# Kernel optimization log

Measured on AMD Instinct MI355X. Metric: run time of the kernel, lower is better.

## Reference

```python
import jax, jax.numpy as jnp
import numpy as np

B, S, F, H = 4, 1024, 256, 8
SCALE = float(F) ** 0.5  # source MULTIPLIES logits by sqrt(f)


def setup_inputs() -> dict:
    key = jax.random.key(0)
    ks = jax.random.split(key, 5)
    # 0.02 init scale keeps sigmoid logits in a non-saturated range
    return {
        "q_input": jax.random.normal(ks[0], (B, S, F), dtype=jnp.float32),
        "Wq": jax.random.normal(ks[1], (F, F * H), dtype=jnp.float32) * 0.02,
        "Wk": jax.random.normal(ks[2], (F, F * H), dtype=jnp.float32) * 0.02,
        "Wv": jax.random.normal(ks[3], (F, F * H), dtype=jnp.float32) * 0.02,
        "Wo": jax.random.normal(ks[4], (F * H, F), dtype=jnp.float32) * 0.02,
    }


def reference(q_input, Wq, Wk, Wv, Wo):
    b, s, f = q_input.shape
    h = Wq.shape[1] // f
    # kv_input is None in source -> self-attention (kv = q_input)
    q = (q_input.reshape(b * s, f) @ Wq).reshape(b, s, f, h)
    k = (q_input.reshape(b * s, f) @ Wk).reshape(b, s, f, h)
    v = (q_input.reshape(b * s, f) @ Wv).reshape(b, s, f, h)
    qkt = jnp.einsum('bifh,bjfh->bijh', q, k)          # [b, i, j, h]
    attn = jax.nn.sigmoid(qkt * SCALE)                  # sigmoid, NOT softmax
    wv = jnp.einsum('bijh,bjfh->bifh', attn, v)         # [b, i, f, h]
    wv = wv.reshape(b * s, f * h)
    out = jax.nn.relu(wv @ Wo)                          # projection + ReLU
    return out.reshape(b, s, f)
```

## Files before the change

### kernel.cpp

```cpp
#include <hip/hip_runtime.h>
#include <math.h>

#define SQ 1024
#define FQ 256
#define FH 2048

typedef _Float16 f16;
typedef f16  f16x8 __attribute__((ext_vector_type(8)));
typedef float f32x4 __attribute__((ext_vector_type(4)));

#define GLOAD_LDS16(gp, lp) \
    __builtin_amdgcn_global_load_lds((const __attribute__((address_space(1))) void*)(gp), \
                                     (__attribute__((address_space(3))) void*)(lp), 16, 0, 0)

#define SIG16(s) __builtin_amdgcn_rcpf(1.0f + __builtin_amdgcn_exp2f(-23.083120654223414f * (s)))

__global__ __launch_bounds__(256) void prep_kernel(const float* __restrict__ x,
                                                   const float* __restrict__ Wq,
                                                   const float* __restrict__ Wk,
                                                   const float* __restrict__ Wv,
                                                   const float* __restrict__ Wo,
                                                   f16* __restrict__ xh,
                                                   f16* __restrict__ wqT,
                                                   f16* __restrict__ wkT,
                                                   f16* __restrict__ wvT,
                                                   f16* __restrict__ woT) {
    const int z = blockIdx.z;
    if (z == 4) {
        int id = (int)(blockIdx.x * 8 + blockIdx.y);
        int idx = (id * 256 + (int)threadIdx.x) * 8;
        float4 a = *(const float4*)(x + idx);
        float4 b = *(const float4*)(x + idx + 4);
        f16x8 v = {(f16)a.x, (f16)a.y, (f16)a.z, (f16)a.w,
                   (f16)b.x, (f16)b.y, (f16)b.z, (f16)b.w};
        *(f16x8*)(xh + idx) = v;
        return;
    }
    __shared__ f16 T[32][33];
    const int tx = threadIdx.x & 31, ty = threadIdx.x >> 5;
    if (z < 3) {
        const float* W = z == 0 ? Wq : (z == 1 ? Wk : Wv);
        f16* WT        = z == 0 ? wqT : (z == 1 ? wkT : wvT);
        const int n0 = blockIdx.x * 32, k0 = blockIdx.y * 32;
#pragma unroll
        for (int i = 0; i < 4; ++i)
            T[ty + i * 8][tx] = (f16)W[(size_t)(k0 + ty + i * 8) * FH + n0 + tx];
        __syncthreads();
#pragma unroll
        for (int i = 0; i < 4; ++i)
            WT[(size_t)(n0 + ty + i * 8) * FQ + k0 + tx] = T[tx][ty + i * 8];
    } else {
        const int n0 = (blockIdx.x >> 3) * 32;
        const int yy = (blockIdx.x & 7) * 8 + blockIdx.y;
        const int ft = yy >> 3, h = yy & 7;
#pragma unroll
        for (int i = 0; i < 4; ++i) {
            int fl = ty + i * 8;
            T[fl][tx] = (f16)Wo[(size_t)((ft * 32 + fl) * 8 + h) * FQ + n0 + tx];
        }
        __syncthreads();
#pragma unroll
        for (int i = 0; i < 4; ++i)
            woT[(size_t)(n0 + ty + i * 8) * FH + h * 256 + ft * 32 + tx] = T[tx][ty + i * 8];
    }
}

__device__ __forceinline__ void stage_sw64(const f16* __restrict__ G, int ldg,
                                           int row0, int c0, f16* S,
                                           int nrows, int w, int lane) {
    const int rsub = lane >> 3;
    const int g    = (lane & 7) ^ (rsub & 7);
#pragma unroll
    for (int rI = w; rI < (nrows >> 3); rI += 4) {
        GLOAD_LDS16(G + (size_t)(row0 + rI * 8 + rsub) * ldg + c0 + g * 8,
                    S + rI * 512);
    }
}

__device__ __forceinline__ void gemm128_sw(const f16* __restrict__ A, int lda,
                                           const f16* __restrict__ Bt, int ldb,
                                           int kbeg, int kend, f16* As, f16* Bs,
                                           f32x4 acc[4][4], int row0, int col0) {
    const int t = threadIdx.x, lane = t & 63, w = t >> 6;
    const int wr = w >> 1, wc = w & 1;
    const int lrow = lane & 15, quad = lane >> 4;
    for (int k0 = kbeg; k0 < kend; k0 += 64) {
        __syncthreads();
        stage_sw64(A, lda, row0, k0, As, 128, w, lane);
        stage_sw64(Bt, ldb, col0, k0, Bs, 128, w, lane);
        __syncthreads();
#pragma unroll
        for (int kk = 0; kk < 2; ++kk) {
            f16x8 af[4], bf[4];
#pragma unroll
            for (int i = 0; i < 4; ++i) {
                int r = wr * 64 + i * 16 + lrow;
                af[i] = *(const f16x8*)&As[r * 64 + (((kk * 4 + quad) ^ (r & 7)) << 3)];
            }
#pragma unroll
            for (int j = 0; j < 4; ++j) {
                int r = wc * 64 + j * 16 + lrow;
                bf[j] = *(const f16x8*)&Bs[r * 64 + (((kk * 4 + quad) ^ (r & 7)) << 3)];
            }
#pragma unroll
            for (int i = 0; i < 4; ++i)
#pragma unroll
                for (int j = 0; j < 4; ++j)
                    acc[i][j] = __builtin_amdgcn_mfma_f32_16x16x32_f16(af[i], bf[j], acc[i][j], 0, 0, 0);
        }
    }
}

__global__ __launch_bounds__(256) void proj_mfma(const f16* __restrict__ xh,
                                                 const f16* __restrict__ wqT,
                                                 const f16* __restrict__ wkT,
                                                 const f16* __restrict__ wvT,
                                                 f16* __restrict__ qb,
                                                 f16* __restrict__ kb,
                                                 f16* __restrict__ vb) {
    const int z = blockIdx.z;
    const f16* WT = z == 0 ? wqT : (z == 1 ? wkT : wvT);
    f16* O        = z == 0 ? qb  : (z == 1 ? kb  : vb);
    __shared__ f16 smem[17408];
    f16* As = smem;
    f16* Bs = smem + 8192;
    f32x4 acc[4][4] = {};
    const int row0 = blockIdx.y * 128, col0 = blockIdx.x * 128;
    gemm128_sw(xh, FQ, WT, FQ, 0, FQ, As, Bs, acc, row0, col0);

    __syncthreads();
    f16* Es = smem;
    const int lane = threadIdx.x & 63, w = threadIdx.x >> 6;
    const int wr = w >> 1, wc = w & 1;
    const int lrow = lane & 15, quad = lane >> 4;
    if (z != 2) {
#pragma unroll
        for (int i = 0; i < 4; ++i)
#pragma unroll
            for (int rr = 0; rr < 4; ++rr) {
                int rl = 64 * wr + 16 * i + 4 * quad + rr;
#pragma unroll
                for (int j = 0; j < 4; ++j) {
                    int cc = 64 * wc + 16 * j + lrow;
                    Es[rl * 136 + (cc & 7) * 16 + (cc >> 3)] = (f16)acc[i][j][rr];
                }
            }
        __syncthreads();
        const int f0 = col0 >> 3;
#pragma unroll
        for (int it = 0; it < 4; ++it) {
            int c = it * 256 + threadIdx.x;
            int row = c >> 3, hh = c & 7;
            int gr = row0 + row, bbb = gr >> 10, s = gr & 1023;
            f16x8 v0 = *(const f16x8*)&Es[row * 136 + hh * 16];
            f16x8 v1 = *(const f16x8*)&Es[row * 136 + hh * 16 + 8];
            f16* dst = O + ((size_t)(bbb * 8 + hh) * SQ + s) * FQ + f0;
            *(f16x8*)dst = v0;
            *(f16x8*)(dst + 8) = v1;
        }
    } else {
#pragma unroll
        for (int i = 0; i < 4; ++i)
#pragma unroll
            for (int rr = 0; rr < 4; ++rr) {
                int rl = 64 * wr + 16 * i + 4 * quad + rr;
#pragma unroll
                for (int j = 0; j < 4; ++j) {
                    int cc = 64 * wc + 16 * j + lrow;
                    Es[cc * 136 + rl] = (f16)acc[i][j][rr];
                }
            }
        __syncthreads();
        const int bbb = row0 >> 10, s0 = row0 & 1023;
#pragma unroll
        for (int it = 0; it < 8; ++it) {
            int c = it * 256 + threadIdx.x;
            int cc = c >> 4, sc = c & 15;
            int hh = cc & 7, f = (col0 >> 3) + (cc >> 3);
            f16x8 v = *(const f16x8*)&Es[cc * 136 + sc * 8];
            *(f16x8*)(O + ((size_t)(bbb * 8 + hh) * FQ + f) * SQ + s0 + sc * 8) = v;
        }
    }
}

__global__ __launch_bounds__(256, 1) void fused_attn(const f16* __restrict__ Qb,
                                                     const f16* __restrict__ Kb,
                                                     const f16* __restrict__ Vt,
                                                     f16* __restrict__ WV) {
    __shared__ f16 smem[37888];
    const int t = threadIdx.x, lane = t & 63, w = t >> 6;
    const int lrow = lane & 15, quad = lane >> 4;
    f16* Pw = smem + 32768 + w * 1280;
    const int n = blockIdx.x;
    const int xcd = n & 7, rest = n >> 3;
    const int bh = xcd * 4 + (rest & 3);
    const int strip = rest >> 2;
    const int m0 = strip * 128;
    const int bb = bh >> 3, h = bh & 7;
    const f16* Qg = Qb + (size_t)bh * SQ * FQ;
    const f16* Kg = Kb + (size_t)bh * SQ * FQ;
    const f16* Vg = Vt + (size_t)bh * FQ * SQ;

    f16x8 qf[2][8];
#pragma unroll
    for (int mi = 0; mi < 2; ++mi)
#pragma unroll
        for (int ks = 0; ks < 8; ++ks)
            qf[mi][ks] = *(const f16x8*)(Qg + (size_t)(m0 + 32 * w + 16 * mi + lrow) * FQ
                                             + ks * 32 + quad * 8);

    const int krs = lane >> 5;
    const int kgp = lane & 31;
    const int vrs = lane >> 2;
    const int vgp = lane & 3;

#pragma unroll
    for (int i = 0; i < 4; ++i) {
        int rI = w + i * 4;
        int r = rI * 2 + krs;
        GLOAD_LDS16(Kg + (size_t)r * FQ + ((kgp ^ (r & 7)) << 3), smem + rI * 512);
    }
#pragma unroll
    for (int i = 0; i < 4; ++i) {
        int rI = w + i * 4;
        int f = rI * 16 + vrs;
        GLOAD_LDS16(Vg + (size_t)f * SQ + ((vgp ^ ((f >> 1) & 3)) << 3),
                    smem + 16384 + rI * 512);
    }

    f32x4 acc_o[2][16] = {};

    for (int jt = 0; jt < 32; ++jt) {
        const int j0 = jt * 32;
        f16* KBc = (jt & 1) ? smem + 8192  : smem;
        f16* VBc = (jt & 1) ? smem + 24576 : smem + 16384;
        __syncthreads();
        if (jt < 31) {
            f16* KBn = (jt & 1) ? smem         : smem + 8192;
            f16* VBn = (jt & 1) ? smem + 16384 : smem + 24576;
#pragma unroll
            for (int i = 0; i < 4; ++i) {
                int rI = w + i * 4;
                int r = rI * 2 + krs;
                GLOAD_LDS16(Kg + (size_t)(j0 + 32 + r) * FQ + ((kgp ^ (r & 7)) << 3),
                            KBn + rI * 512);
            }
#pragma unroll
            for (int i = 0; i < 4; ++i) {
                int rI = w + i * 4;
                int f = rI * 16 + vrs;
                GLOAD_LDS16(Vg + (size_t)f * SQ + j0 + 32 + ((vgp ^ ((f >> 1) & 3)) << 3),
                            VBn + rI * 512);
            }
        }
        f32x4 acc_s[2][2] = {};
#pragma unroll
        for (int ks = 0; ks < 8; ++ks) {
            f16x8 bf[2];
#pragma unroll
            for (int nj = 0; nj < 2; ++nj) {
                int rk = 16 * nj + lrow;
                bf[nj] = *(const f16x8*)&KBc[rk * 256 + (((ks * 4 + quad) ^ (rk & 7)) << 3)];
            }
#pragma unroll
            for (int mi = 0; mi < 2; ++mi)
#pragma unroll
                for (int nj = 0; nj < 2; ++nj)
                    acc_s[mi][nj] = __builtin_amdgcn_mfma_f32_16x16x32_f16(
                        qf[mi][ks], bf[nj], acc_s[mi][nj], 0, 0, 0);
        }
#pragma unroll
        for (int mi = 0; mi < 2; ++mi)
#pragma unroll
            for (int nj = 0; nj < 2; ++nj)
#pragma unroll
                for (int rr = 0; rr < 4; ++rr)
                    Pw[(16 * mi + 4 * quad + rr) * 40 + 16 * nj + lrow] =
                        (f16)SIG16(acc_s[mi][nj][rr]);
        f16x8 ap[2];
#pragma unroll
        for (int mi = 0; mi < 2; ++mi)
            ap[mi] = *(const f16x8*)&Pw[(16 * mi + lrow) * 40 + quad * 8];
#pragma unroll
        for (int nj = 0; nj < 16; ++nj) {
            int f = 16 * nj + lrow;
            f16x8 bv = *(const f16x8*)&VBc[f * 32 + ((quad ^ ((f >> 1) & 3)) << 3)];
#pragma unroll
            for (int mi = 0; mi < 2; ++mi)
                acc_o[mi][nj] = __builtin_amdgcn_mfma_f32_16x16x32_f16(
                    ap[mi], bv, acc_o[mi][nj], 0, 0, 0);
        }
    }
    __syncthreads();
    f16* Es = smem;
#pragma unroll
    for (int mi = 0; mi < 2; ++mi)
#pragma unroll
        for (int nj = 0; nj < 16; ++nj)
#pragma unroll
            for (int rr = 0; rr < 4; ++rr)
                Es[(32 * w + 16 * mi + 4 * quad + rr) * 264 + 16 * nj + lrow] =
                    (f16)acc_o[mi][nj][rr];
    __syncthreads();
#pragma unroll
    for (int it = 0; it < 16; ++it) {
        int c = it * 256 + t;
        int r = c >> 5, ck = c & 31;
        f16x8 v = *(const f16x8*)&Es[r * 264 + ck * 8];
        *(f16x8*)(WV + (size_t)(bb * SQ + m0 + r) * FH + h * 256 + ck * 8) = v;
    }
}

__global__ __launch_bounds__(256) void out_mfma8(const f16* __restrict__ WVm,
                                                 const f16* __restrict__ WoT,
                                                 float* __restrict__ PP) {
    __shared__ f16 smem[16384];
    f16* As = smem;
    f16* Bs = smem + 8192;
    f32x4 acc[4][4] = {};
    const int row0 = blockIdx.y * 128, col0 = blockIdx.x * 128;
    const int kbeg = blockIdx.z * 256;
    gemm128_sw(WVm, FH, WoT, FH, kbeg, kbeg + 256, As, Bs, acc, row0, col0);

    float* P = PP + (size_t)blockIdx.z * SQ * 4 * FQ;
    const int lane = threadIdx.x & 63, w = threadIdx.x >> 6;
    const int wr = w >> 1, wc = w & 1;
    const int lrow = lane & 15, quad = lane >> 4;
#pragma unroll
    for (int i = 0; i < 4; ++i)
#pragma unroll
        for (int rr = 0; rr < 4; ++rr) {
            int gr = row0 + wr * 64 + i * 16 + quad * 4 + rr;
#pragma unroll
            for (int j = 0; j < 4; ++j) {
                int gc = col0 + wc * 64 + j * 16 + lrow;
                P[(size_t)gr * FQ + gc] = acc[i][j][rr];
            }
        }
}

__global__ __launch_bounds__(256) void reduce_relu8(const float* __restrict__ PP,
                                                    float* __restrict__ O) {
    int idx = (blockIdx.x * 256 + threadIdx.x) * 4;
    f32x4 s = *(const f32x4*)(PP + idx);
#pragma unroll
    for (int z = 1; z < 8; ++z)
        s += *(const f32x4*)(PP + (size_t)z * 1048576 + idx);
    f32x4 r = {fmaxf(s.x, 0.f), fmaxf(s.y, 0.f), fmaxf(s.z, 0.f), fmaxf(s.w, 0.f)};
    *(f32x4*)(O + idx) = r;
}

extern "C" void kernel_launch(void* const* d_in, const int* in_sizes, int n_in,
                              void* d_out, int out_size, void* d_ws, size_t ws_size,
                              hipStream_t stream) {
    const float* x  = (const float*)d_in[0];
    const float* Wq = (const float*)d_in[1];
    const float* Wk = (const float*)d_in[2];
    const float* Wv = (const float*)d_in[3];
    const float* Wo = (const float*)d_in[4];
    float* out = (float*)d_out;

    f16* ws = (f16*)d_ws;
    f16* xh    = ws;
    f16* wqT   = xh    + 1048576;
    f16* wkT   = wqT   + 524288;
    f16* wvT   = wkT   + 524288;
    f16* woT   = wvT   + 524288;
    f16* qbuf  = woT   + 524288;
    f16* kbuf  = qbuf  + 8388608;
    f16* vbuf  = kbuf  + 8388608;
    f16* wvbuf = vbuf  + 8388608;
    float* pp  = (float*)qbuf;

    dim3 blk(256);
    prep_kernel<<<dim3(64, 8, 5), blk, 0, stream>>>(x, Wq, Wk, Wv, Wo,
                                                    xh, wqT, wkT, wvT, woT);

    proj_mfma<<<dim3(16, 32, 3), blk, 0, stream>>>(xh, wqT, wkT, wvT, qbuf, kbuf, vbuf);

    fused_attn<<<dim3(256), blk, 0, stream>>>(qbuf, kbuf, vbuf, wvbuf);

    out_mfma8<<<dim3(2, 32, 8), blk, 0, stream>>>(wvbuf, woT, pp);
    reduce_relu8<<<dim3(1024), blk, 0, stream>>>(pp, out);
}
```

Measured before the change: 181.8 us.

## Split attention KV loop across two warp groups with cross-group reduction

The attention kernel now runs 512 threads per block as two 4-wave groups. Each group processes alternating 32-key tiles of every 64-key step, so a block works on two tiles per iteration and halves the loop trip count. Group 0 loads K and group 1 loads V for both tiles. At the end, group 1 writes its partial fp32 output accumulators to LDS and group 0 adds them before the fp16 store. This doubles the waves per CU to hide latency, at the cost of doubled LDS, a reduction step and more per-thread register pressure under the launch bound of 2.

New measurement: 161.3 us. 1.13x faster.

```diff
diff --git a/kernel.cpp b/kernel.cpp
--- a/kernel.cpp
+++ b/kernel.cpp
@@ -183,14 +183,15 @@
     }
 }
 
-__global__ __launch_bounds__(256, 1) void fused_attn(const f16* __restrict__ Qb,
+__global__ __launch_bounds__(512, 2) void fused_attn(const f16* __restrict__ Qb,
                                                      const f16* __restrict__ Kb,
                                                      const f16* __restrict__ Vt,
                                                      f16* __restrict__ WV) {
-    __shared__ f16 smem[37888];
+    __shared__ f16 smem[75776];
     const int t = threadIdx.x, lane = t & 63, w = t >> 6;
+    const int grp = w >> 2, wl = w & 3;
     const int lrow = lane & 15, quad = lane >> 4;
-    f16* Pw = smem + 32768 + w * 1280;
+    f16* Pw = smem + 65536 + w * 1280;
     const int n = blockIdx.x;
     const int xcd = n & 7, rest = n >> 3;
     const int bh = xcd * 4 + (rest & 3);
@@ -206,7 +207,7 @@
     for (int mi = 0; mi < 2; ++mi)
 #pragma unroll
         for (int ks = 0; ks < 8; ++ks)
-            qf[mi][ks] = *(const f16x8*)(Qg + (size_t)(m0 + 32 * w + 16 * mi + lrow) * FQ
+            qf[mi][ks] = *(const f16x8*)(Qg + (size_t)(m0 + 32 * wl + 16 * mi + lrow) * FQ
                                              + ks * 32 + quad * 8);
 
     const int krs = lane >> 5;
@@ -214,43 +215,58 @@
     const int vrs = lane >> 2;
     const int vgp = lane & 3;
 
-#pragma unroll
-    for (int i = 0; i < 4; ++i) {
-        int rI = w + i * 4;
-        int r = rI * 2 + krs;
-        GLOAD_LDS16(Kg + (size_t)r * FQ + ((kgp ^ (r & 7)) << 3), smem + rI * 512);
-    }
-#pragma unroll
-    for (int i = 0; i < 4; ++i) {
-        int rI = w + i * 4;
-        int f = rI * 16 + vrs;
-        GLOAD_LDS16(Vg + (size_t)f * SQ + ((vgp ^ ((f >> 1) & 3)) << 3),
-                    smem + 16384 + rI * 512);
+    if (grp == 0) {
+#pragma unroll
+        for (int kt = 0; kt < 2; ++kt)
+#pragma unroll
+            for (int i = 0; i < 4; ++i) {
+                int rI = wl + i * 4;
+                int r = rI * 2 + krs;
+                GLOAD_LDS16(Kg + (size_t)(kt * 32 + r) * FQ + ((kgp ^ (r & 7)) << 3),
+                            smem + kt * 8192 + rI * 512);
+            }
+    } else {
+#pragma unroll
+        for (int kt = 0; kt < 2; ++kt)
+#pragma unroll
+            for (int i = 0; i < 4; ++i) {
+                int rI = wl + i * 4;
+                int f = rI * 16 + vrs;
+                GLOAD_LDS16(Vg + (size_t)f * SQ + kt * 32 + ((vgp ^ ((f >> 1) & 3)) << 3),
+                            smem + 32768 + kt * 8192 + rI * 512);
+            }
     }
 
     f32x4 acc_o[2][16] = {};
 
-    for (int jt = 0; jt < 32; ++jt) {
-        const int j0 = jt * 32;
-        f16* KBc = (jt & 1) ? smem + 8192  : smem;
-        f16* VBc = (jt & 1) ? smem + 24576 : smem + 16384;
-        __syncthreads();
-        if (jt < 31) {
-            f16* KBn = (jt & 1) ? smem         : smem + 8192;
-            f16* VBn = (jt & 1) ? smem + 16384 : smem + 24576;
-#pragma unroll
-            for (int i = 0; i < 4; ++i) {
-                int rI = w + i * 4;
-                int r = rI * 2 + krs;
-                GLOAD_LDS16(Kg + (size_t)(j0 + 32 + r) * FQ + ((kgp ^ (r & 7)) << 3),
-                            KBn + rI * 512);
-            }
-#pragma unroll
-            for (int i = 0; i < 4; ++i) {
-                int rI = w + i * 4;
-                int f = rI * 16 + vrs;
-                GLOAD_LDS16(Vg + (size_t)f * SQ + j0 + 32 + ((vgp ^ ((f >> 1) & 3)) << 3),
-                            VBn + rI * 512);
+    for (int it = 0; it < 16; ++it) {
+        const int p = it & 1;
+        f16* KBc = smem + (p * 2 + grp) * 8192;
+        f16* VBc = smem + 32768 + (p * 2 + grp) * 8192;
+        __syncthreads();
+        if (it < 15) {
+            const int pn = p ^ 1;
+            const int base = (it + 1) * 64;
+            if (grp == 0) {
+#pragma unroll
+                for (int kt = 0; kt < 2; ++kt)
+#pragma unroll
+                    for (int i = 0; i < 4; ++i) {
+                        int rI = wl + i * 4;
+                        int r = rI * 2 + krs;
+                        GLOAD_LDS16(Kg + (size_t)(base + kt * 32 + r) * FQ + ((kgp ^ (r & 7)) << 3),
+                                    smem + (pn * 2 + kt) * 8192 + rI * 512);
+                    }
+            } else {
+#pragma unroll
+                for (int kt = 0; kt < 2; ++kt)
+#pragma unroll
+                    for (int i = 0; i < 4; ++i) {
+                        int rI = wl + i * 4;
+                        int f = rI * 16 + vrs;
+                        GLOAD_LDS16(Vg + (size_t)f * SQ + base + kt * 32 + ((vgp ^ ((f >> 1) & 3)) << 3),
+                                    smem + 32768 + (pn * 2 + kt) * 8192 + rI * 512);
+                    }
             }
         }
         f32x4 acc_s[2][2] = {};
@@ -292,19 +308,32 @@
         }
     }
     __syncthreads();
+    float* Fb = (float*)(smem + 34816);
     f16* Es = smem;
 #pragma unroll
-    for (int mi = 0; mi < 2; ++mi)
-#pragma unroll
-        for (int nj = 0; nj < 16; ++nj)
-#pragma unroll
-            for (int rr = 0; rr < 4; ++rr)
-                Es[(32 * w + 16 * mi + 4 * quad + rr) * 264 + 16 * nj + lrow] =
-                    (f16)acc_o[mi][nj][rr];
-    __syncthreads();
-#pragma unroll
-    for (int it = 0; it < 16; ++it) {
-        int c = it * 256 + t;
+    for (int mi = 0; mi < 2; ++mi) {
+        if (grp == 1) {
+#pragma unroll
+            for (int nj = 0; nj < 16; ++nj)
+                *(f32x4*)&Fb[((wl * 16 + nj) << 8) + lane * 4] = acc_o[mi][nj];
+        }
+        __syncthreads();
+        if (grp == 0) {
+#pragma unroll
+            for (int nj = 0; nj < 16; ++nj) {
+                f32x4 s = acc_o[mi][nj] +
+                          *(const f32x4*)&Fb[((wl * 16 + nj) << 8) + lane * 4];
+#pragma unroll
+                for (int rr = 0; rr < 4; ++rr)
+                    Es[(32 * wl + 16 * mi + 4 * quad + rr) * 264 + 16 * nj + lrow] =
+                        (f16)s[rr];
+            }
+        }
+        __syncthreads();
+    }
+#pragma unroll
+    for (int it = 0; it < 8; ++it) {
+        int c = it * 512 + t;
         int r = c >> 5, ck = c & 31;
         f16x8 v = *(const f16x8*)&Es[r * 264 + ck * 8];
         *(f16x8*)(WV + (size_t)(bb * SQ + m0 + r) * FH + h * 256 + ck * 8) = v;
@@ -378,7 +407,7 @@
 
     proj_mfma<<<dim3(16, 32, 3), blk, 0, stream>>>(xh, wqT, wkT, wvT, qbuf, kbuf, vbuf);
 
-    fused_attn<<<dim3(256), blk, 0, stream>>>(qbuf, kbuf, vbuf, wvbuf);
+    fused_attn<<<dim3(256), dim3(512), 0, stream>>>(qbuf, kbuf, vbuf, wvbuf);
 
     out_mfma8<<<dim3(2, 32, 8), blk, 0, stream>>>(wvbuf, woT, pp);
     reduce_relu8<<<dim3(1024), blk, 0, stream>>>(pp, out);
```
